# Performance work log

Hardware: AMD Instinct MI355X
Metric: run time of the kernel (lower is better)

The kernel has to match this reference:

```python
import jax, jax.numpy as jnp
import numpy as np

GROUPS = 16
EPS = 1e-5


def _dcn_v2(x, offset, mask, weight):
    """Modulated deformable 3x3 conv, stride=1, pad=1, no bias.
    x: [B,C,H,W], offset: [B,18,H,W] (dy,dx interleaved per kernel point),
    mask: [B,9,H,W] (modulation scalars), weight: [O,C,3,3]."""
    B, C, H, W = x.shape
    O = weight.shape[0]
    K = 9
    # kernel-point displacements, row-major (kh, kw): k = kh*3 + kw
    ky = jnp.repeat(jnp.arange(3) - 1, 3).astype(x.dtype)   # [9]
    kx = jnp.tile(jnp.arange(3) - 1, 3).astype(x.dtype)      # [9]
    dy = offset[:, 0::2]  # [B,9,H,W]
    dx = offset[:, 1::2]  # [B,9,H,W]
    hh = jnp.arange(H, dtype=x.dtype)
    ww = jnp.arange(W, dtype=x.dtype)
    # sampling coordinates (stride=1, pad=1)
    ys = hh[None, None, :, None] + ky[None, :, None, None] + dy  # [B,9,H,W]
    xs = ww[None, None, None, :] + kx[None, :, None, None] + dx  # [B,9,H,W]

    y0 = jnp.floor(ys)
    x0 = jnp.floor(xs)
    wy1 = ys - y0
    wx1 = xs - x0
    y0i = y0.astype(jnp.int32)
    x0i = x0.astype(jnp.int32)

    flat = x.reshape(B, C, H * W)

    def gather(yi, xi, w):
        # yi, xi, w: [B,9,H,W]; zero-padding outside the image
        valid = (yi >= 0) & (yi < H) & (xi >= 0) & (xi < W)
        idx = jnp.clip(yi, 0, H - 1) * W + jnp.clip(xi, 0, W - 1)  # [B,9,H,W]
        g = jnp.take_along_axis(flat, idx.reshape(B, 1, K * H * W), axis=2)
        g = g.reshape(B, C, K, H, W)
        return g * (w * valid.astype(x.dtype))[:, None]  # [B,C,9,H,W]

    val = (gather(y0i,     x0i,     (1 - wy1) * (1 - wx1))
         + gather(y0i,     x0i + 1, (1 - wy1) * wx1)
         + gather(y0i + 1, x0i,     wy1 * (1 - wx1))
         + gather(y0i + 1, x0i + 1, wy1 * wx1))
    val = val * mask[:, None]  # modulation
    # implicit GEMM: [B,C,9,H,W] x [O,C,9] -> [B,O,H,W]
    return jnp.einsum('bckhw,ock->bohw', val, weight.reshape(O, C, K))


def _group_norm(x, gamma, beta):
    B, C, H, W = x.shape
    xg = x.reshape(B, GROUPS, C // GROUPS, H, W)
    mu = xg.mean(axis=(2, 3, 4), keepdims=True)
    var = xg.var(axis=(2, 3, 4), keepdims=True)
    xn = ((xg - mu) * jax.lax.rsqrt(var + EPS)).reshape(B, C, H, W)
    return xn * gamma[None, :, None, None] + beta[None, :, None, None]


def setup_inputs() -> dict:
    key = jax.random.key(0)
    k1, k2, k3, k4 = jax.random.split(key, 4)
    B, C, O, H, W = 8, 256, 256, 64, 64
    x = jax.random.normal(k1, (B, C, H, W), dtype=jnp.float32)
    offset = jax.random.normal(k2, (B, 18, H, W), dtype=jnp.float32)
    mask = jax.random.uniform(k3, (B, 9, H, W), dtype=jnp.float32)
    weight = jax.random.normal(k4, (O, C, 3, 3), dtype=jnp.float32) * (1.0 / np.sqrt(C * 9))
    gamma = jnp.ones((O,), dtype=jnp.float32)
    beta = jnp.zeros((O,), dtype=jnp.float32)
    return {"x": x, "offset": offset, "mask": mask, "weight": weight,
            "gamma": gamma, "beta": beta}


def reference(x, offset, mask, weight, gamma, beta):
    out = _dcn_v2(x, offset, mask, weight)
    return _group_norm(out, gamma, beta)
```

## Files before the change

### kernel.cpp

```cpp
#include <hip/hip_runtime.h>
#include <stdint.h>


#define B_ 8
#define C_ 256
#define O_ 256
#define H_ 64
#define W_ 64
#define HW_ 4096
#define KTOT 2304
#define GROUPS_ 16
#define EPS_ 1e-5f
#define NSTEP 36
#define VROW 72

typedef float  f32x4  __attribute__((ext_vector_type(4)));
typedef short  short8 __attribute__((ext_vector_type(8)));
typedef unsigned int   u32;
typedef unsigned short u16;

#define XT_BYTES (B_*HW_*C_*2)
#define WIMG_OFF  XT_BYTES
#define WIMG_BYTES (72*16*64*16)
#define STATS_OFF (WIMG_OFF + WIMG_BYTES)

__device__ __forceinline__ u32 bf16r(float f) {
    u32 u = __float_as_uint(f);
    return (u + 0x7fffu + ((u >> 16) & 1u)) >> 16;
}
__device__ __forceinline__ u32 pack_bf16x2(float lo, float hi) {
    return bf16r(lo) | (bf16r(hi) << 16);
}
__device__ __forceinline__ u32 pack_trunc(float lo, float hi) {
    return (__float_as_uint(hi) & 0xffff0000u) | (__float_as_uint(lo) >> 16);
}
__device__ __forceinline__ float bflo(u32 u) { return __uint_as_float(u << 16); }
__device__ __forceinline__ float bfhi(u32 u) { return __uint_as_float(u & 0xffff0000u); }

__device__ __forceinline__ void barrier_lds() {
    asm volatile("s_waitcnt lgkmcnt(0)\n\ts_barrier" ::: "memory");
}

__global__ void k_prep(const float* __restrict__ x, u16* __restrict__ xt,
                       const float* __restrict__ w, u16* __restrict__ wimg) {
    const int bid = blockIdx.x;
    const int tid = threadIdx.x;
    if (bid < 2048) {
        __shared__ float tile[64][65];
        const int b = bid >> 8, ct = (bid >> 6) & 3, pt = bid & 63;
#pragma unroll
        for (int pass = 0; pass < 4; ++pass) {
            const int r  = (tid >> 4) + pass * 16;
            const int pq = tid & 15;
            const f32x4 v = *(const f32x4*)&x[(((size_t)(b * C_ + ct * 64 + r)) << 12)
                                              + pt * 64 + pq * 4];
            tile[r][pq * 4 + 0] = v.x;
            tile[r][pq * 4 + 1] = v.y;
            tile[r][pq * 4 + 2] = v.z;
            tile[r][pq * 4 + 3] = v.w;
        }
        __syncthreads();
        const int pr = tid >> 2, cg = tid & 3;
        u32 o[8];
#pragma unroll
        for (int j = 0; j < 8; ++j)
            o[j] = pack_bf16x2(tile[cg * 16 + 2 * j][pr], tile[cg * 16 + 2 * j + 1][pr]);
        u16* dst = &xt[(((size_t)b << 12) + pt * 64 + pr) * 256 + ct * 64 + cg * 16];
        *(uint4*)dst       = *(uint4*)&o[0];
        *(uint4*)(dst + 8) = *(uint4*)&o[4];
    } else {
        const int sub = bid - 2048;
        const int k  = sub >> 3;
        const int c0 = (sub & 7) * 32;
#pragma unroll
        for (int i = 0; i < 4; ++i) {
            const int item = tid + i * 256;
            const int lane = item & 63;
            const int frag = item >> 6;
            const int col = lane & 15, quad = lane >> 4;
            const int n = frag * 16 + col;
            const float* src = w + (size_t)n * KTOT + (size_t)(c0 + quad * 8) * 9 + k;
            u32 o[4];
#pragma unroll
            for (int j = 0; j < 4; ++j)
                o[j] = pack_bf16x2(src[(size_t)(2 * j) * 9], src[(size_t)(2 * j + 1) * 9]);
            *(uint4*)&wimg[((size_t)sub * 1024 + item) * 8] = *(uint4*)o;
        }
    }
}

__device__ __forceinline__ void issue_gather(const u16* __restrict__ cb,
                                             const float* __restrict__ mwp,
                                             const int* __restrict__ mip,
                                             int gpos, uint4 g[8], f32x4& mw) {
    mw = *(const f32x4*)&mwp[gpos * 4];
    const int4 ix = *(const int4*)&mip[gpos * 4];
    const u16* p0 = cb + ix.x;
    const u16* p1 = cb + ix.y;
    const u16* p2 = cb + ix.z;
    const u16* p3 = cb + ix.w;
    g[0] = *(const uint4*)p0; g[1] = *(const uint4*)(p0 + 8);
    g[2] = *(const uint4*)p1; g[3] = *(const uint4*)(p1 + 8);
    g[4] = *(const uint4*)p2; g[5] = *(const uint4*)(p2 + 8);
    g[6] = *(const uint4*)p3; g[7] = *(const uint4*)(p3 + 8);
}

__device__ __forceinline__ void interp_store(const uint4 g[8], f32x4 mw, u16* dst) {
    float s[16];
#pragma unroll
    for (int i = 0; i < 16; ++i) s[i] = 0.f;
    const float ww[4] = {mw.x, mw.y, mw.z, mw.w};
#pragma unroll
    for (int cr = 0; cr < 4; ++cr) {
        const float wg = ww[cr];
        const uint4 a = g[2 * cr], bq = g[2 * cr + 1];
        s[0]  += wg * bflo(a.x);  s[1]  += wg * bfhi(a.x);
        s[2]  += wg * bflo(a.y);  s[3]  += wg * bfhi(a.y);
        s[4]  += wg * bflo(a.z);  s[5]  += wg * bfhi(a.z);
        s[6]  += wg * bflo(a.w);  s[7]  += wg * bfhi(a.w);
        s[8]  += wg * bflo(bq.x); s[9]  += wg * bfhi(bq.x);
        s[10] += wg * bflo(bq.y); s[11] += wg * bfhi(bq.y);
        s[12] += wg * bflo(bq.z); s[13] += wg * bfhi(bq.z);
        s[14] += wg * bflo(bq.w); s[15] += wg * bfhi(bq.w);
    }
    uint4 pk0, pk1;
    pk0.x = pack_trunc(s[0], s[1]);   pk0.y = pack_trunc(s[2], s[3]);
    pk0.z = pack_trunc(s[4], s[5]);   pk0.w = pack_trunc(s[6], s[7]);
    pk1.x = pack_trunc(s[8], s[9]);   pk1.y = pack_trunc(s[10], s[11]);
    pk1.z = pack_trunc(s[12], s[13]); pk1.w = pack_trunc(s[14], s[15]);
    *(uint4*)dst = pk0;
    *(uint4*)(dst + 8) = pk1;
}

__device__ __forceinline__ void load_wfrags(const u16* __restrict__ wimg, int s,
                                            int wid, int lane, short8 bf[8]) {
#pragma unroll
    for (int kc = 0; kc < 2; ++kc)
#pragma unroll
        for (int ni = 0; ni < 4; ++ni)
            bf[kc * 4 + ni] = *(const short8*)
                &wimg[(((size_t)(2 * s + kc) * 16 + wid * 4 + ni) * 64 + lane) * 8];
}

__launch_bounds__(256, 2)
__global__ void k_dcn(const u16* __restrict__ xt, const u16* __restrict__ wimg,
                      const float* __restrict__ offp, const float* __restrict__ mskp,
                      float* __restrict__ out, float* __restrict__ stats) {
    __shared__ __align__(16) float meta_w[9 * 64 * 4];
    __shared__ __align__(16) int   meta_i[9 * 64 * 4];
    __shared__ __align__(16) u16   lds_v[2][64 * VROW];

    const int tid = threadIdx.x;
    const int gid = blockIdx.x;
    const int b   = gid & 7;
    const int m0  = (gid >> 3) * 64;
    const int lane = tid & 63, wid = tid >> 6;
    const int col = lane & 15, quad = lane >> 4;
    const int gpos = tid >> 2, oct = tid & 3;

    const u16* xtb = xt + ((size_t)b << 20);

    for (int it = tid; it < 576; it += 256) {
        const int pos = it & 63, k = it >> 6;
        const int pg = m0 + pos;
        const int hh = pg >> 6, wwi = pg & 63;
        const float dy = offp[((size_t)(b * 18 + 2 * k) << 12) + pg];
        const float dx = offp[((size_t)(b * 18 + 2 * k + 1) << 12) + pg];
        const float mv = mskp[((size_t)(b * 9 + k) << 12) + pg];
        const float ys = (float)(hh + (k / 3) - 1) + dy;
        const float xs = (float)(wwi + (k % 3) - 1) + dx;
        const float y0f = floorf(ys), x0f = floorf(xs);
        const int y0 = (int)y0f, x0 = (int)x0f;
        const float wy1 = ys - y0f, wx1 = xs - x0f;
        const float wy0 = 1.f - wy1, wx0 = 1.f - wx1;
        const int y1 = y0 + 1, x1 = x0 + 1;
        const float vy0 = (y0 >= 0 && y0 < H_) ? 1.f : 0.f;
        const float vy1 = (y1 >= 0 && y1 < H_) ? 1.f : 0.f;
        const float vx0 = (x0 >= 0 && x0 < W_) ? 1.f : 0.f;
        const float vx1 = (x1 >= 0 && x1 < W_) ? 1.f : 0.f;
        const int y0c = min(max(y0, 0), H_ - 1), y1c = min(max(y1, 0), H_ - 1);
        const int x0c = min(max(x0, 0), W_ - 1), x1c = min(max(x1, 0), W_ - 1);
        meta_w[it * 4 + 0] = mv * wy0 * wx0 * vy0 * vx0;
        meta_w[it * 4 + 1] = mv * wy0 * wx1 * vy0 * vx1;
        meta_w[it * 4 + 2] = mv * wy1 * wx0 * vy1 * vx0;
        meta_w[it * 4 + 3] = mv * wy1 * wx1 * vy1 * vx1;
        meta_i[it * 4 + 0] = (y0c * W_ + x0c) << 8;
        meta_i[it * 4 + 1] = (y0c * W_ + x1c) << 8;
        meta_i[it * 4 + 2] = (y1c * W_ + x0c) << 8;
        meta_i[it * 4 + 3] = (y1c * W_ + x1c) << 8;
    }
    __syncthreads();

    uint4 g[8]; f32x4 mw; short8 bf_cur[8], bf_nxt[8];
    issue_gather(xtb + 0 + oct * 16, &meta_w[0], &meta_i[0], gpos, g, mw);
    load_wfrags(wimg, 0, wid, lane, bf_cur);
    interp_store(g, mw, &lds_v[0][gpos * VROW + oct * 16]);
    __syncthreads();

    f32x4 acc[4][4];
#pragma unroll
    for (int i = 0; i < 4; ++i)
#pragma unroll
        for (int j = 0; j < 4; ++j) acc[i][j] = (f32x4){0.f, 0.f, 0.f, 0.f};

#pragma unroll 2
    for (int s = 0; s < NSTEP; ++s) {
        const int p = s & 1;
        const bool pf = (s + 1 < NSTEP);

        if (pf) load_wfrags(wimg, s + 1, wid, lane, bf_nxt);

        if (pf) {
            const int sn = s + 1;
            const int kn = sn >> 2, c0n = (sn & 3) * 64;
            issue_gather(xtb + c0n + oct * 16, &meta_w[kn * 256], &meta_i[kn * 256],
                         gpos, g, mw);
        }

#pragma unroll
        for (int kc = 0; kc < 2; ++kc) {
            short8 af[4];
#pragma unroll
            for (int mi = 0; mi < 4; ++mi)
                af[mi] = *(const short8*)
                    &lds_v[p][(mi * 16 + col) * VROW + kc * 32 + quad * 8];
#pragma unroll
            for (int mi = 0; mi < 4; ++mi)
#pragma unroll
                for (int ni = 0; ni < 4; ++ni)
                    acc[mi][ni] = __builtin_amdgcn_mfma_f32_16x16x32_bf16(
                        af[mi], bf_cur[kc * 4 + ni], acc[mi][ni], 0, 0, 0);
        }

        if (pf) interp_store(g, mw, &lds_v[1 - p][gpos * VROW + oct * 16]);

        barrier_lds();

#pragma unroll
        for (int i = 0; i < 8; ++i) bf_cur[i] = bf_nxt[i];
    }

#pragma unroll
    for (int mi = 0; mi < 4; ++mi)
#pragma unroll
        for (int ni = 0; ni < 4; ++ni) {
            const int o  = wid * 64 + ni * 16 + col;
            const int pg = m0 + mi * 16 + quad * 4;
            *(f32x4*)(out + (((size_t)b * O_ + o) << 12) + pg) = acc[mi][ni];
        }

#pragma unroll
    for (int ni = 0; ni < 4; ++ni) {
        float s = 0.f, s2 = 0.f;
#pragma unroll
        for (int mi = 0; mi < 4; ++mi) {
            f32x4 v = acc[mi][ni];
            s  += v.x + v.y + v.z + v.w;
            s2 += v.x * v.x + v.y * v.y + v.z * v.z + v.w * v.w;
        }
#pragma unroll
        for (int d = 32; d > 0; d >>= 1) {
            s  += __shfl_xor(s, d, 64);
            s2 += __shfl_xor(s2, d, 64);
        }
        if (lane == 0) {
            const int gI = wid * 4 + ni;
            atomicAdd(&stats[b * GROUPS_ + gI], s);
            atomicAdd(&stats[128 + b * GROUPS_ + gI], s2);
        }
    }
}

__global__ void k_gn(float* __restrict__ out, const float* __restrict__ stats,
                     const float* __restrict__ gamma, const float* __restrict__ beta) {
    const int blk = blockIdx.x;
    const int b = blk >> 8, o = blk & 255;
    const int gI = b * GROUPS_ + (o >> 4);
    const float n = 65536.f;
    const float mean = stats[gI] / n;
    const float var  = stats[128 + gI] / n - mean * mean;
    const float inv  = rsqrtf(fmaxf(var, 0.f) + EPS_);
    const float scale = inv * gamma[o];
    const float shift = beta[o] - mean * scale;
    f32x4* p = (f32x4*)(out + ((size_t)blk << 12));
    const int t = threadIdx.x;
#pragma unroll
    for (int i = 0; i < 4; ++i) {
        f32x4 v = p[t + i * 256];
        p[t + i * 256] = v * scale + shift;
    }
}

extern "C" void kernel_launch(void* const* d_in, const int* in_sizes, int n_in,
                              void* d_out, int out_size, void* d_ws, size_t ws_size,
                              hipStream_t stream) {
    const float* x     = (const float*)d_in[0];
    const float* offp  = (const float*)d_in[1];
    const float* mskp  = (const float*)d_in[2];
    const float* w     = (const float*)d_in[3];
    const float* gamma = (const float*)d_in[4];
    const float* beta  = (const float*)d_in[5];
    float* outp = (float*)d_out;

    u16*   xt    = (u16*)d_ws;
    u16*   wimg  = (u16*)((char*)d_ws + WIMG_OFF);
    float* stats = (float*)((char*)d_ws + STATS_OFF);

    hipMemsetAsync(stats, 0, 1024, stream);
    k_prep<<<dim3(2048 + 72), dim3(256), 0, stream>>>(x, xt, w, wimg);
    k_dcn<<<dim3(512), dim3(256), 0, stream>>>(xt, wimg, offp, mskp, outp, stats);
    k_gn<<<dim3(2048), dim3(256), 0, stream>>>(outp, stats, gamma, beta);
}
```

Before: 193.8 us.

## Split DCN reduction dimension in two halves and combine with sum-of-squares pass

The deformable-conv GEMM kernel now splits its 36-step K loop into two halves across twice as many blocks, writing partial outputs to the final buffer and a workspace buffer. A new kernel adds the partials and computes the sum of squares for group norm, while the DCN kernel still accumulates plain sums atomically. Launch bounds rise to 4 blocks per SM and the bf16 packing uses a byte-permute instruction. This aims to fill more CUs with 1024 blocks in exchange for an extra full read/write pass over the output and higher register pressure.

```diff
diff --git a/kernel.cpp b/kernel.cpp
--- a/kernel.cpp
+++ b/kernel.cpp
@@ -19,10 +19,12 @@
 typedef unsigned int   u32;
 typedef unsigned short u16;
 
-#define XT_BYTES (B_*HW_*C_*2)
-#define WIMG_OFF  XT_BYTES
+#define XT_BYTES   (B_*HW_*C_*2)
+#define WIMG_OFF   XT_BYTES
 #define WIMG_BYTES (72*16*64*16)
-#define STATS_OFF (WIMG_OFF + WIMG_BYTES)
+#define STATS_OFF  (WIMG_OFF + WIMG_BYTES)
+#define PART_OFF   (STATS_OFF + 1024)
+#define WS_NEED    (PART_OFF + (size_t)B_*O_*HW_*4)
 
 __device__ __forceinline__ u32 bf16r(float f) {
     u32 u = __float_as_uint(f);
@@ -31,11 +33,11 @@
 __device__ __forceinline__ u32 pack_bf16x2(float lo, float hi) {
     return bf16r(lo) | (bf16r(hi) << 16);
 }
-__device__ __forceinline__ u32 pack_trunc(float lo, float hi) {
-    return (__float_as_uint(hi) & 0xffff0000u) | (__float_as_uint(lo) >> 16);
+__device__ __forceinline__ u32 pack_perm(float lo, float hi) {
+    return __builtin_amdgcn_perm(__float_as_uint(hi), __float_as_uint(lo), 0x07060302u);
 }
 __device__ __forceinline__ float bflo(u32 u) { return __uint_as_float(u << 16); }
-__device__ __forceinline__ float bfhi(u32 u) { return __uint_as_float(u & 0xffff0000u); }
+__device__ __forceinline__ float bfhi_f(u32 u) { return __uint_as_float(u); }
 
 __device__ __forceinline__ void barrier_lds() {
     asm volatile("s_waitcnt lgkmcnt(0)\n\ts_barrier" ::: "memory");
@@ -114,20 +116,20 @@
     for (int cr = 0; cr < 4; ++cr) {
         const float wg = ww[cr];
         const uint4 a = g[2 * cr], bq = g[2 * cr + 1];
-        s[0]  += wg * bflo(a.x);  s[1]  += wg * bfhi(a.x);
-        s[2]  += wg * bflo(a.y);  s[3]  += wg * bfhi(a.y);
-        s[4]  += wg * bflo(a.z);  s[5]  += wg * bfhi(a.z);
-        s[6]  += wg * bflo(a.w);  s[7]  += wg * bfhi(a.w);
-        s[8]  += wg * bflo(bq.x); s[9]  += wg * bfhi(bq.x);
-        s[10] += wg * bflo(bq.y); s[11] += wg * bfhi(bq.y);
-        s[12] += wg * bflo(bq.z); s[13] += wg * bfhi(bq.z);
-        s[14] += wg * bflo(bq.w); s[15] += wg * bfhi(bq.w);
+        s[0]  += wg * bflo(a.x);  s[1]  += wg * bfhi_f(a.x);
+        s[2]  += wg * bflo(a.y);  s[3]  += wg * bfhi_f(a.y);
+        s[4]  += wg * bflo(a.z);  s[5]  += wg * bfhi_f(a.z);
+        s[6]  += wg * bflo(a.w);  s[7]  += wg * bfhi_f(a.w);
+        s[8]  += wg * bflo(bq.x); s[9]  += wg * bfhi_f(bq.x);
+        s[10] += wg * bflo(bq.y); s[11] += wg * bfhi_f(bq.y);
+        s[12] += wg * bflo(bq.z); s[13] += wg * bfhi_f(bq.z);
+        s[14] += wg * bflo(bq.w); s[15] += wg * bfhi_f(bq.w);
     }
     uint4 pk0, pk1;
-    pk0.x = pack_trunc(s[0], s[1]);   pk0.y = pack_trunc(s[2], s[3]);
-    pk0.z = pack_trunc(s[4], s[5]);   pk0.w = pack_trunc(s[6], s[7]);
-    pk1.x = pack_trunc(s[8], s[9]);   pk1.y = pack_trunc(s[10], s[11]);
-    pk1.z = pack_trunc(s[12], s[13]); pk1.w = pack_trunc(s[14], s[15]);
+    pk0.x = pack_perm(s[0], s[1]);   pk0.y = pack_perm(s[2], s[3]);
+    pk0.z = pack_perm(s[4], s[5]);   pk0.w = pack_perm(s[6], s[7]);
+    pk1.x = pack_perm(s[8], s[9]);   pk1.y = pack_perm(s[10], s[11]);
+    pk1.z = pack_perm(s[12], s[13]); pk1.w = pack_perm(s[14], s[15]);
     *(uint4*)dst = pk0;
     *(uint4*)(dst + 8) = pk1;
 }
@@ -142,10 +144,11 @@
                 &wimg[(((size_t)(2 * s + kc) * 16 + wid * 4 + ni) * 64 + lane) * 8];
 }
 
-__launch_bounds__(256, 2)
+__launch_bounds__(256, 4)
 __global__ void k_dcn(const u16* __restrict__ xt, const u16* __restrict__ wimg,
                       const float* __restrict__ offp, const float* __restrict__ mskp,
-                      float* __restrict__ out, float* __restrict__ stats) {
+                      float* __restrict__ out0, float* __restrict__ out1,
+                      float* __restrict__ stats, int half_len) {
     __shared__ __align__(16) float meta_w[9 * 64 * 4];
     __shared__ __align__(16) int   meta_i[9 * 64 * 4];
     __shared__ __align__(16) u16   lds_v[2][64 * VROW];
@@ -153,15 +156,21 @@
     const int tid = threadIdx.x;
     const int gid = blockIdx.x;
     const int b   = gid & 7;
-    const int m0  = (gid >> 3) * 64;
+    const int m0  = ((gid >> 3) & 63) * 64;
+    const int half = gid >> 9;
+    const int s0 = half * half_len, s1 = s0 + half_len;
+    const int klo = s0 >> 2;
+    const int kcnt = ((s1 - 1) >> 2) - klo + 1;
+    float* outbuf = half ? out1 : out0;
+
     const int lane = tid & 63, wid = tid >> 6;
     const int col = lane & 15, quad = lane >> 4;
     const int gpos = tid >> 2, oct = tid & 3;
 
     const u16* xtb = xt + ((size_t)b << 20);
 
-    for (int it = tid; it < 576; it += 256) {
-        const int pos = it & 63, k = it >> 6;
+    for (int it = tid; it < 64 * kcnt; it += 256) {
+        const int pos = it & 63, k = klo + (it >> 6);
         const int pg = m0 + pos;
         const int hh = pg >> 6, wwi = pg & 63;
         const float dy = offp[((size_t)(b * 18 + 2 * k) << 12) + pg];
@@ -192,8 +201,12 @@
     __syncthreads();
 
     uint4 g[8]; f32x4 mw; short8 bf_cur[8], bf_nxt[8];
-    issue_gather(xtb + 0 + oct * 16, &meta_w[0], &meta_i[0], gpos, g, mw);
-    load_wfrags(wimg, 0, wid, lane, bf_cur);
+    {
+        const int kn = s0 >> 2, c0 = (s0 & 3) * 64;
+        issue_gather(xtb + c0 + oct * 16, &meta_w[(kn - klo) * 256],
+                     &meta_i[(kn - klo) * 256], gpos, g, mw);
+    }
+    load_wfrags(wimg, s0, wid, lane, bf_cur);
     interp_store(g, mw, &lds_v[0][gpos * VROW + oct * 16]);
     __syncthreads();
 
@@ -204,17 +217,18 @@
         for (int j = 0; j < 4; ++j) acc[i][j] = (f32x4){0.f, 0.f, 0.f, 0.f};
 
 #pragma unroll 2
-    for (int s = 0; s < NSTEP; ++s) {
-        const int p = s & 1;
-        const bool pf = (s + 1 < NSTEP);
+    for (int i = 0; i < half_len; ++i) {
+        const int s = s0 + i;
+        const int p = i & 1;
+        const bool pf = (i + 1 < half_len);
 
         if (pf) load_wfrags(wimg, s + 1, wid, lane, bf_nxt);
 
         if (pf) {
             const int sn = s + 1;
             const int kn = sn >> 2, c0n = (sn & 3) * 64;
-            issue_gather(xtb + c0n + oct * 16, &meta_w[kn * 256], &meta_i[kn * 256],
-                         gpos, g, mw);
+            issue_gather(xtb + c0n + oct * 16, &meta_w[(kn - klo) * 256],
+                         &meta_i[(kn - klo) * 256], gpos, g, mw);
         }
 
 #pragma unroll
@@ -237,7 +251,7 @@
         barrier_lds();
 
 #pragma unroll
-        for (int i = 0; i < 8; ++i) bf_cur[i] = bf_nxt[i];
+        for (int j = 0; j < 8; ++j) bf_cur[j] = bf_nxt[j];
     }
 
 #pragma unroll
@@ -246,7 +260,7 @@
         for (int ni = 0; ni < 4; ++ni) {
             const int o  = wid * 64 + ni * 16 + col;
             const int pg = m0 + mi * 16 + quad * 4;
-            *(f32x4*)(out + (((size_t)b * O_ + o) << 12) + pg) = acc[mi][ni];
+            *(f32x4*)(outbuf + (((size_t)b * O_ + o) << 12) + pg) = acc[mi][ni];
         }
 
 #pragma unroll
@@ -256,19 +270,61 @@
         for (int mi = 0; mi < 4; ++mi) {
             f32x4 v = acc[mi][ni];
             s  += v.x + v.y + v.z + v.w;
-            s2 += v.x * v.x + v.y * v.y + v.z * v.z + v.w * v.w;
-        }
-#pragma unroll
-        for (int d = 32; d > 0; d >>= 1) {
-            s  += __shfl_xor(s, d, 64);
-            s2 += __shfl_xor(s2, d, 64);
-        }
+        }
+#pragma unroll
+        for (int d = 32; d > 0; d >>= 1) s += __shfl_xor(s, d, 64);
         if (lane == 0) {
             const int gI = wid * 4 + ni;
             atomicAdd(&stats[b * GROUPS_ + gI], s);
-            atomicAdd(&stats[128 + b * GROUPS_ + gI], s2);
-        }
-    }
+        }
+        (void)s2;
+    }
+}
+
+__global__ void k_sumsq(const float* __restrict__ out0, const float* __restrict__ out1,
+                        float* __restrict__ outsum, float* __restrict__ stats) {
+    const int blk = blockIdx.x;
+    const int b = blk >> 8, o = blk & 255;
+    const int t = threadIdx.x;
+    const f32x4* p0 = (const f32x4*)(out0 + ((size_t)blk << 12));
+    const f32x4* p1 = (const f32x4*)(out1 + ((size_t)blk << 12));
+    f32x4* po = (f32x4*)(outsum + ((size_t)blk << 12));
+    float s2 = 0.f;
+#pragma unroll
+    for (int i = 0; i < 4; ++i) {
+        f32x4 v = p0[t + i * 256] + p1[t + i * 256];
+        po[t + i * 256] = v;
+        s2 += v.x * v.x + v.y * v.y + v.z * v.z + v.w * v.w;
+    }
+#pragma unroll
+    for (int d = 32; d > 0; d >>= 1) s2 += __shfl_xor(s2, d, 64);
+    __shared__ float red[4];
+    if ((t & 63) == 0) red[t >> 6] = s2;
+    __syncthreads();
+    if (t == 0)
+        atomicAdd(&stats[128 + b * GROUPS_ + (o >> 4)],
+                  red[0] + red[1] + red[2] + red[3]);
+}
+
+__global__ void k_sumsq1(const float* __restrict__ out0, float* __restrict__ stats) {
+    const int blk = blockIdx.x;
+    const int b = blk >> 8, o = blk & 255;
+    const int t = threadIdx.x;
+    const f32x4* p0 = (const f32x4*)(out0 + ((size_t)blk << 12));
+    float s2 = 0.f;
+#pragma unroll
+    for (int i = 0; i < 4; ++i) {
+        f32x4 v = p0[t + i * 256];
+        s2 += v.x * v.x + v.y * v.y + v.z * v.z + v.w * v.w;
+    }
+#pragma unroll
+    for (int d = 32; d > 0; d >>= 1) s2 += __shfl_xor(s2, d, 64);
+    __shared__ float red[4];
+    if ((t & 63) == 0) red[t >> 6] = s2;
+    __syncthreads();
+    if (t == 0)
+        atomicAdd(&stats[128 + b * GROUPS_ + (o >> 4)],
+                  red[0] + red[1] + red[2] + red[3]);
 }
 
 __global__ void k_gn(float* __restrict__ out, const float* __restrict__ stats,
@@ -305,9 +361,18 @@
     u16*   xt    = (u16*)d_ws;
     u16*   wimg  = (u16*)((char*)d_ws + WIMG_OFF);
     float* stats = (float*)((char*)d_ws + STATS_OFF);
+    float* part  = (float*)((char*)d_ws + PART_OFF);
 
     hipMemsetAsync(stats, 0, 1024, stream);
     k_prep<<<dim3(2048 + 72), dim3(256), 0, stream>>>(x, xt, w, wimg);
-    k_dcn<<<dim3(512), dim3(256), 0, stream>>>(xt, wimg, offp, mskp, outp, stats);
+    if (ws_size >= WS_NEED) {
+        k_dcn<<<dim3(1024), dim3(256), 0, stream>>>(xt, wimg, offp, mskp,
+                                                    outp, part, stats, NSTEP / 2);
+        k_sumsq<<<dim3(2048), dim3(256), 0, stream>>>(outp, part, outp, stats);
+    } else {
+        k_dcn<<<dim3(512), dim3(256), 0, stream>>>(xt, wimg, offp, mskp,
+                                                   outp, part, stats, NSTEP);
+        k_sumsq1<<<dim3(2048), dim3(256), 0, stream>>>(outp, stats);
+    }
     k_gn<<<dim3(2048), dim3(256), 0, stream>>>(outp, stats, gamma, beta);
 }
```

Result: slower. 488.4 us (+152.0%).

## Prefetch deformable gathers two steps ahead and spread weight prep over more blocks

Applied to the files above, without the earlier changes.

The main loop now issues each bilinear gather two steps ahead into a double-buffered register set, so global-load latency is hidden behind two MFMA steps instead of one. Bilinear accumulation drops the mask on the high bf16 half, and packing uses a single byte-permute instruction. The weight-reformat part of the prep kernel gives one item per thread across four times as many blocks. The deeper prefetch doubles the live gather registers, which under launch_bounds(256,2) may cause spills or pressure; reading the high half unmasked leaves low-mantissa bits in the products, a small numeric change.

```diff
diff --git a/kernel.cpp b/kernel.cpp
--- a/kernel.cpp
+++ b/kernel.cpp
@@ -19,10 +19,10 @@
 typedef unsigned int   u32;
 typedef unsigned short u16;
 
-#define XT_BYTES (B_*HW_*C_*2)
-#define WIMG_OFF  XT_BYTES
+#define XT_BYTES   (B_*HW_*C_*2)
+#define WIMG_OFF   XT_BYTES
 #define WIMG_BYTES (72*16*64*16)
-#define STATS_OFF (WIMG_OFF + WIMG_BYTES)
+#define STATS_OFF  (WIMG_OFF + WIMG_BYTES)
 
 __device__ __forceinline__ u32 bf16r(float f) {
     u32 u = __float_as_uint(f);
@@ -31,11 +31,11 @@
 __device__ __forceinline__ u32 pack_bf16x2(float lo, float hi) {
     return bf16r(lo) | (bf16r(hi) << 16);
 }
-__device__ __forceinline__ u32 pack_trunc(float lo, float hi) {
-    return (__float_as_uint(hi) & 0xffff0000u) | (__float_as_uint(lo) >> 16);
+__device__ __forceinline__ u32 pack_perm(float lo, float hi) {
+    return __builtin_amdgcn_perm(__float_as_uint(hi), __float_as_uint(lo), 0x07060302u);
 }
 __device__ __forceinline__ float bflo(u32 u) { return __uint_as_float(u << 16); }
-__device__ __forceinline__ float bfhi(u32 u) { return __uint_as_float(u & 0xffff0000u); }
+__device__ __forceinline__ float bfhi_f(u32 u) { return __uint_as_float(u); }
 
 __device__ __forceinline__ void barrier_lds() {
     asm volatile("s_waitcnt lgkmcnt(0)\n\ts_barrier" ::: "memory");
@@ -69,14 +69,14 @@
         *(uint4*)dst       = *(uint4*)&o[0];
         *(uint4*)(dst + 8) = *(uint4*)&o[4];
     } else {
-        const int sub = bid - 2048;
-        const int k  = sub >> 3;
-        const int c0 = (sub & 7) * 32;
-#pragma unroll
-        for (int i = 0; i < 4; ++i) {
-            const int item = tid + i * 256;
-            const int lane = item & 63;
-            const int frag = item >> 6;
+        const int item = (bid - 2048) * 256 + tid;
+        if (item < 72 * 1024) {
+            const int sub = item >> 10;
+            const int idx = item & 1023;
+            const int k  = sub >> 3;
+            const int c0 = (sub & 7) * 32;
+            const int lane = idx & 63;
+            const int frag = idx >> 6;
             const int col = lane & 15, quad = lane >> 4;
             const int n = frag * 16 + col;
             const float* src = w + (size_t)n * KTOT + (size_t)(c0 + quad * 8) * 9 + k;
@@ -84,7 +84,7 @@
 #pragma unroll
             for (int j = 0; j < 4; ++j)
                 o[j] = pack_bf16x2(src[(size_t)(2 * j) * 9], src[(size_t)(2 * j + 1) * 9]);
-            *(uint4*)&wimg[((size_t)sub * 1024 + item) * 8] = *(uint4*)o;
+            *(uint4*)&wimg[((size_t)sub * 1024 + idx) * 8] = *(uint4*)o;
         }
     }
 }
@@ -114,20 +114,20 @@
     for (int cr = 0; cr < 4; ++cr) {
         const float wg = ww[cr];
         const uint4 a = g[2 * cr], bq = g[2 * cr + 1];
-        s[0]  += wg * bflo(a.x);  s[1]  += wg * bfhi(a.x);
-        s[2]  += wg * bflo(a.y);  s[3]  += wg * bfhi(a.y);
-        s[4]  += wg * bflo(a.z);  s[5]  += wg * bfhi(a.z);
-        s[6]  += wg * bflo(a.w);  s[7]  += wg * bfhi(a.w);
-        s[8]  += wg * bflo(bq.x); s[9]  += wg * bfhi(bq.x);
-        s[10] += wg * bflo(bq.y); s[11] += wg * bfhi(bq.y);
-        s[12] += wg * bflo(bq.z); s[13] += wg * bfhi(bq.z);
-        s[14] += wg * bflo(bq.w); s[15] += wg * bfhi(bq.w);
+        s[0]  += wg * bflo(a.x);  s[1]  += wg * bfhi_f(a.x);
+        s[2]  += wg * bflo(a.y);  s[3]  += wg * bfhi_f(a.y);
+        s[4]  += wg * bflo(a.z);  s[5]  += wg * bfhi_f(a.z);
+        s[6]  += wg * bflo(a.w);  s[7]  += wg * bfhi_f(a.w);
+        s[8]  += wg * bflo(bq.x); s[9]  += wg * bfhi_f(bq.x);
+        s[10] += wg * bflo(bq.y); s[11] += wg * bfhi_f(bq.y);
+        s[12] += wg * bflo(bq.z); s[13] += wg * bfhi_f(bq.z);
+        s[14] += wg * bflo(bq.w); s[15] += wg * bfhi_f(bq.w);
     }
     uint4 pk0, pk1;
-    pk0.x = pack_trunc(s[0], s[1]);   pk0.y = pack_trunc(s[2], s[3]);
-    pk0.z = pack_trunc(s[4], s[5]);   pk0.w = pack_trunc(s[6], s[7]);
-    pk1.x = pack_trunc(s[8], s[9]);   pk1.y = pack_trunc(s[10], s[11]);
-    pk1.z = pack_trunc(s[12], s[13]); pk1.w = pack_trunc(s[14], s[15]);
+    pk0.x = pack_perm(s[0], s[1]);   pk0.y = pack_perm(s[2], s[3]);
+    pk0.z = pack_perm(s[4], s[5]);   pk0.w = pack_perm(s[6], s[7]);
+    pk1.x = pack_perm(s[8], s[9]);   pk1.y = pack_perm(s[10], s[11]);
+    pk1.z = pack_perm(s[12], s[13]); pk1.w = pack_perm(s[14], s[15]);
     *(uint4*)dst = pk0;
     *(uint4*)(dst + 8) = pk1;
 }
@@ -191,10 +191,11 @@
     }
     __syncthreads();
 
-    uint4 g[8]; f32x4 mw; short8 bf_cur[8], bf_nxt[8];
-    issue_gather(xtb + 0 + oct * 16, &meta_w[0], &meta_i[0], gpos, g, mw);
+    uint4 g2[2][8]; f32x4 mw2[2]; short8 bf_cur[8], bf_nxt[8];
+    issue_gather(xtb + 0 + oct * 16, &meta_w[0], &meta_i[0], gpos, g2[0], mw2[0]);
     load_wfrags(wimg, 0, wid, lane, bf_cur);
-    interp_store(g, mw, &lds_v[0][gpos * VROW + oct * 16]);
+    interp_store(g2[0], mw2[0], &lds_v[0][gpos * VROW + oct * 16]);
+    issue_gather(xtb + 64 + oct * 16, &meta_w[0], &meta_i[0], gpos, g2[1], mw2[1]);
     __syncthreads();
 
     f32x4 acc[4][4];
@@ -206,15 +207,14 @@
 #pragma unroll 2
     for (int s = 0; s < NSTEP; ++s) {
         const int p = s & 1;
-        const bool pf = (s + 1 < NSTEP);
-
-        if (pf) load_wfrags(wimg, s + 1, wid, lane, bf_nxt);
-
-        if (pf) {
-            const int sn = s + 1;
+
+        if (s + 1 < NSTEP) load_wfrags(wimg, s + 1, wid, lane, bf_nxt);
+
+        if (s + 2 < NSTEP) {
+            const int sn = s + 2;
             const int kn = sn >> 2, c0n = (sn & 3) * 64;
             issue_gather(xtb + c0n + oct * 16, &meta_w[kn * 256], &meta_i[kn * 256],
-                         gpos, g, mw);
+                         gpos, g2[p], mw2[p]);
         }
 
 #pragma unroll
@@ -232,12 +232,13 @@
                         af[mi], bf_cur[kc * 4 + ni], acc[mi][ni], 0, 0, 0);
         }
 
-        if (pf) interp_store(g, mw, &lds_v[1 - p][gpos * VROW + oct * 16]);
+        if (s + 1 < NSTEP)
+            interp_store(g2[1 - p], mw2[1 - p], &lds_v[1 - p][gpos * VROW + oct * 16]);
 
         barrier_lds();
 
 #pragma unroll
-        for (int i = 0; i < 8; ++i) bf_cur[i] = bf_nxt[i];
+        for (int j = 0; j < 8; ++j) bf_cur[j] = bf_nxt[j];
     }
 
 #pragma unroll
@@ -307,7 +308,7 @@
     float* stats = (float*)((char*)d_ws + STATS_OFF);
 
     hipMemsetAsync(stats, 0, 1024, stream);
-    k_prep<<<dim3(2048 + 72), dim3(256), 0, stream>>>(x, xt, w, wimg);
+    k_prep<<<dim3(2048 + 288), dim3(256), 0, stream>>>(x, xt, w, wimg);
     k_dcn<<<dim3(512), dim3(256), 0, stream>>>(xt, wimg, offp, mskp, outp, stats);
     k_gn<<<dim3(2048), dim3(256), 0, stream>>>(outp, stats, gamma, beta);
 }
```

Result: faster. 185.8 us (-4.1%).
